# Kernel optimization log

Measured on AMD Instinct MI355X. Metric: run time of the kernel, lower is better.

The kernel has to match this reference:

```python
import jax, jax.numpy as jnp
import numpy as np

D_MODEL, H, D_FF = 1024, 16, 4096
D_K = D_MODEL // H
EPS = 1e-5


def _layernorm(x, alpha, bias):
    # faithful to source: unbiased std (ddof=1), eps added to std (not var)
    mean = jnp.mean(x, axis=-1, keepdims=True)
    std = jnp.std(x, axis=-1, keepdims=True, ddof=1)
    return alpha * (x - mean) / (std + EPS) + bias


def setup_inputs() -> dict:
    key = jax.random.key(0)
    ks = jax.random.split(key, 12)
    B, S = 2, 2048
    s = 1.0 / np.sqrt(D_MODEL)
    inp = {
        "x": jax.random.normal(ks[0], (B, S, D_MODEL), dtype=jnp.float32),
        "mask": jnp.ones((B, 1, 1, S), dtype=jnp.int32),
        "wq": jax.random.normal(ks[1], (D_MODEL, D_MODEL), dtype=jnp.float32) * s,
        "wk": jax.random.normal(ks[2], (D_MODEL, D_MODEL), dtype=jnp.float32) * s,
        "wv": jax.random.normal(ks[3], (D_MODEL, D_MODEL), dtype=jnp.float32) * s,
        "wo": jax.random.normal(ks[4], (D_MODEL, D_MODEL), dtype=jnp.float32) * s,
        "w1": jax.random.normal(ks[5], (D_MODEL, D_FF), dtype=jnp.float32) * s,
        "b1": jnp.zeros((D_FF,), dtype=jnp.float32),
        "w2": jax.random.normal(ks[6], (D_FF, D_MODEL), dtype=jnp.float32) * (1.0 / np.sqrt(D_FF)),
        "b2": jnp.zeros((D_MODEL,), dtype=jnp.float32),
        "alpha1": jnp.ones((1,), dtype=jnp.float32),
        "bias1": jnp.zeros((1,), dtype=jnp.float32),
        "alpha2": jnp.ones((1,), dtype=jnp.float32),
        "bias2": jnp.zeros((1,), dtype=jnp.float32),
    }
    return inp


def reference(x, mask, wq, wk, wv, wo, w1, b1, w2, b2, alpha1, bias1, alpha2, bias2):
    B, S, _ = x.shape

    # --- sublayer 1: pre-norm self-attention + residual ---
    xn = _layernorm(x, alpha1, bias1)
    q = (xn @ wq).reshape(B, S, H, D_K).transpose(0, 2, 1, 3)  # [B,H,S,Dk]
    k = (xn @ wk).reshape(B, S, H, D_K).transpose(0, 2, 1, 3)
    v = (xn @ wv).reshape(B, S, H, D_K).transpose(0, 2, 1, 3)

    scores = jnp.einsum("bhqd,bhkd->bhqk", q, k) / np.sqrt(D_K)  # [B,H,S,S]
    scores = jnp.where(mask == 0, jnp.float32(-1e9), scores)
    attn = jax.nn.softmax(scores, axis=-1)
    ctx = jnp.einsum("bhqk,bhkd->bhqd", attn, v)
    ctx = ctx.transpose(0, 2, 1, 3).reshape(B, S, D_MODEL)
    x = x + ctx @ wo

    # --- sublayer 2: pre-norm FFN + residual ---
    xn = _layernorm(x, alpha2, bias2)
    h = jax.nn.relu(xn @ w1 + b1)
    x = x + h @ w2 + b2
    return x
```

## Files before the change

kernel.cpp:

```cpp
#include <hip/hip_runtime.h>
#include <hip/hip_bf16.h>

typedef __attribute__((ext_vector_type(8))) short bf16x8;
typedef __attribute__((ext_vector_type(4))) short short4v;
typedef __attribute__((ext_vector_type(4))) float floatx4;

#define MFMA16(A, B, C) __builtin_amdgcn_mfma_f32_16x16x32_bf16((A), (B), (C), 0, 0, 0)

__device__ inline short bf16bits(float f) {
  __hip_bfloat16 h = __float2bfloat16(f);
  return *reinterpret_cast<short*>(&h);
}
__device__ inline unsigned cvtpk(float lo, float hi) {
  unsigned r;
  asm("v_cvt_pk_bf16_f32 %0, %1, %2" : "=v"(r) : "v"(lo), "v"(hi));
  return r;
}
typedef __attribute__((address_space(3))) char lds_char;
typedef __attribute__((address_space(1))) const char glob_char;
__device__ inline void gll16(const void* g, void* l) {
  __builtin_amdgcn_global_load_lds((glob_char*)g, (lds_char*)l, 16, 0, 0);
}

__global__ __launch_bounds__(256) void transpose_qkv_kernel(
    const float* __restrict__ wq, const float* __restrict__ wk,
    const float* __restrict__ wv, __hip_bfloat16* __restrict__ wqkvT) {
  __shared__ __align__(16) __hip_bfloat16 tile[64][72];
  const int which = blockIdx.y >> 4;
  const float* src = which == 0 ? wq : (which == 1 ? wk : wv);
  __hip_bfloat16* dst = wqkvT + (size_t)which * 1024 * 1024;
  const long r0 = (long)(blockIdx.y & 15) * 64, c0 = (long)blockIdx.x * 64;
  for (int i = threadIdx.x; i < 1024; i += 256) {
    int r = i >> 4, c4 = (i & 15) * 4;
    float4 f = *(const float4*)&src[(r0 + r) * 1024 + c0 + c4];
    short4v s;
    s[0] = bf16bits(f.x); s[1] = bf16bits(f.y);
    s[2] = bf16bits(f.z); s[3] = bf16bits(f.w);
    *(short4v*)&tile[r][c4] = s;
  }
  __syncthreads();
  for (int i = threadIdx.x; i < 512; i += 256) {
    int c = i >> 3, r8 = (i & 7) * 8;
    bf16x8 sv;
#pragma unroll
    for (int j = 0; j < 8; j++) sv[j] = *reinterpret_cast<const short*>(&tile[r8 + j][c]);
    *(bf16x8*)&dst[(c0 + c) * 1024 + r0 + r8] = sv;
  }
}

__global__ __launch_bounds__(256) void prep_kernel(
    const __hip_bfloat16* __restrict__ qkv, __hip_bfloat16* __restrict__ vt,
    const float* __restrict__ wo, __hip_bfloat16* __restrict__ woT,
    const int* __restrict__ mask, float* __restrict__ addm,
    int* __restrict__ flags) {
  __shared__ __align__(16) __hip_bfloat16 tile[64][72];
  __shared__ int ok[4];
  const int bid = blockIdx.x;
  if (bid < 1024) {
    const int bh = bid >> 5, b = bh >> 4, h = bh & 15;
    const long s0 = (long)(bid & 31) * 64;
    const __hip_bfloat16* src = qkv + ((long)b * 2048 + s0) * 3072 + 2048 + h * 64;
    for (int i = threadIdx.x; i < 512; i += 256) {
      int s = i >> 3, d8 = (i & 7) * 8;
      *(uint4*)&tile[s][d8] = *(const uint4*)&src[(long)s * 3072 + d8];
    }
    __syncthreads();
    __hip_bfloat16* dstb = vt + (long)bh * 64 * 2048 + s0;
    for (int i = threadIdx.x; i < 512; i += 256) {
      int d = i >> 3, s8 = (i & 7) * 8;
      bf16x8 sv;
#pragma unroll
      for (int j = 0; j < 8; j++) sv[j] = *reinterpret_cast<const short*>(&tile[s8 + j][d]);
      *(bf16x8*)&dstb[(long)d * 2048 + s8] = sv;
    }
  } else if (bid < 1280) {
    const int t = bid - 1024;
    const long r0 = (long)(t >> 4) * 64, c0 = (long)(t & 15) * 64;
    for (int i = threadIdx.x; i < 1024; i += 256) {
      int r = i >> 4, c4 = (i & 15) * 4;
      float4 f = *(const float4*)&wo[(r0 + r) * 1024 + c0 + c4];
      short4v s;
      s[0] = bf16bits(f.x); s[1] = bf16bits(f.y);
      s[2] = bf16bits(f.z); s[3] = bf16bits(f.w);
      *(short4v*)&tile[r][c4] = s;
    }
    __syncthreads();
    for (int i = threadIdx.x; i < 512; i += 256) {
      int c = i >> 3, r8 = (i & 7) * 8;
      bf16x8 sv;
#pragma unroll
      for (int j = 0; j < 8; j++) sv[j] = *reinterpret_cast<const short*>(&tile[r8 + j][c]);
      *(bf16x8*)&woT[(c0 + c) * 1024 + r0 + r8] = sv;
    }
  } else {
    const int i = (bid - 1280) * 256 + threadIdx.x;
    const int mv = mask[i];
    addm[i] = mv ? 0.f : -1e30f;
    const unsigned long long bal = __ballot(mv != 0);
    if ((threadIdx.x & 63) == 0) ok[threadIdx.x >> 6] = (bal == ~0ull) ? 1 : 0;
    __syncthreads();
    if (threadIdx.x == 0) flags[bid - 1280] = ok[0] & ok[1] & ok[2] & ok[3];
  }
}

__global__ __launch_bounds__(256) void wtrans_kernel(
    const float* __restrict__ w1c, const float* __restrict__ w2c,
    __hip_bfloat16* __restrict__ w1Th, __hip_bfloat16* __restrict__ w2Th) {
  __shared__ __align__(16) __hip_bfloat16 tile[64][72];
  const int bid = blockIdx.x;
  const float* src;
  __hip_bfloat16* dst;
  int R, ldS;
  long r0, c0;
  if (bid < 512) {
    src = w1c; dst = w1Th; R = 1024; ldS = 4096;
    r0 = (long)(bid >> 5) * 64; c0 = (long)(bid & 31) * 64;
  } else {
    const int t = bid - 512;
    src = w2c; dst = w2Th; R = 2048; ldS = 1024;
    r0 = (long)(t >> 4) * 64; c0 = (long)(t & 15) * 64;
  }
  for (int i = threadIdx.x; i < 1024; i += 256) {
    int r = i >> 4, c4 = (i & 15) * 4;
    float4 f = *(const float4*)&src[(r0 + r) * ldS + c0 + c4];
    short4v s;
    s[0] = bf16bits(f.x); s[1] = bf16bits(f.y);
    s[2] = bf16bits(f.z); s[3] = bf16bits(f.w);
    *(short4v*)&tile[r][c4] = s;
  }
  __syncthreads();
  for (int i = threadIdx.x; i < 512; i += 256) {
    int c = i >> 3, r8 = (i & 7) * 8;
    bf16x8 sv;
#pragma unroll
    for (int j = 0; j < 8; j++) sv[j] = *reinterpret_cast<const short*>(&tile[r8 + j][c]);
    *(bf16x8*)&dst[(c0 + c) * R + r0 + r8] = sv;
  }
}

__global__ __launch_bounds__(256) void bias_add_kernel(
    const float* __restrict__ x1, const float* __restrict__ b2,
    float* __restrict__ out) {
  const int i = (blockIdx.x * 256 + threadIdx.x) * 4;
  float4 v = *(const float4*)&x1[i];
  const float4 bb = *(const float4*)&b2[i & 1023];
  v.x += bb.x; v.y += bb.y; v.z += bb.z; v.w += bb.w;
  *(float4*)&out[i] = v;
}

__global__ __launch_bounds__(256) void ln_kernel(
    const float* __restrict__ x, __hip_bfloat16* __restrict__ y,
    const float* __restrict__ alpha_p, const float* __restrict__ bias_p) {
  __shared__ float sred[8];
  const long row = blockIdx.x;
  const int t = threadIdx.x;
  const float* xr = x + row * 1024;
  float v[4];
#pragma unroll
  for (int i = 0; i < 4; i++) v[i] = xr[t * 4 + i];
  float sum = 0.f, sq = 0.f;
#pragma unroll
  for (int i = 0; i < 4; i++) { sum += v[i]; sq += v[i] * v[i]; }
#pragma unroll
  for (int off = 32; off; off >>= 1) {
    sum += __shfl_down(sum, off);
    sq += __shfl_down(sq, off);
  }
  if ((t & 63) == 0) { sred[(t >> 6) * 2] = sum; sred[(t >> 6) * 2 + 1] = sq; }
  __syncthreads();
  sum = sred[0] + sred[2] + sred[4] + sred[6];
  sq = sred[1] + sred[3] + sred[5] + sred[7];
  const float mean = sum * (1.f / 1024.f);
  float var = (sq - 1024.f * mean * mean) * (1.f / 1023.f);
  var = fmaxf(var, 0.f);
  const float denom = sqrtf(var) + 1e-5f;
  const float sc = alpha_p[0] / denom;
  const float beta = bias_p[0];
  __hip_bfloat16* yr = y + row * 1024;
#pragma unroll
  for (int i = 0; i < 4; i++) yr[t * 4 + i] = __float2bfloat16((v[i] - mean) * sc + beta);
}

template <int EPI>
__global__ __launch_bounds__(256) void gemm_bt_kernel(
    const __hip_bfloat16* __restrict__ A, const __hip_bfloat16* __restrict__ Bt,
    void* __restrict__ Cv, const float* __restrict__ bias,
    const float* __restrict__ res, int M, int N, int K) {
  __shared__ __align__(16) __hip_bfloat16 lA[2][128 * 32];
  __shared__ __align__(16) __hip_bfloat16 lB[2][128 * 32];
  const int tid = threadIdx.x;
  const int wave = tid >> 6, lane = tid & 63;
  const int quad = lane >> 4, l16 = lane & 15;
  const int wm = wave >> 1, wn = wave & 1;

  const int gx = gridDim.x;
  const int nwg = gx * gridDim.y;
  int bid = blockIdx.y * gx + blockIdx.x;
  bid = (bid & 7) * (nwg >> 3) + (bid >> 3);
  const long m0 = (long)(bid / gx) * 128;
  const long n0 = (long)(bid % gx) * 128;

  const int rA0 = tid >> 2, cA0 = (tid & 3) * 8;
  const int rA1 = (tid + 256) >> 2, cA1 = ((tid + 256) & 3) * 8;

  floatx4 acc[4][4];
#pragma unroll
  for (int i = 0; i < 4; i++)
#pragma unroll
    for (int j = 0; j < 4; j++) acc[i][j] = (floatx4){0.f, 0.f, 0.f, 0.f};

  const __hip_bfloat16* Ab = A + m0 * K;
  const __hip_bfloat16* Bb = Bt + n0 * K;

  gll16(&Ab[(long)rA0 * K + cA0], &lA[0][wave * 512]);
  gll16(&Ab[(long)rA1 * K + cA1], &lA[0][2048 + wave * 512]);
  gll16(&Bb[(long)rA0 * K + cA0], &lB[0][wave * 512]);
  gll16(&Bb[(long)rA1 * K + cA1], &lB[0][2048 + wave * 512]);

  int cur = 0;
  for (int k0 = 0; k0 < K; k0 += 32) {
    __syncthreads();
    if (k0 + 32 < K) {
      const int nxt = cur ^ 1;
      gll16(&Ab[(long)rA0 * K + k0 + 32 + cA0], &lA[nxt][wave * 512]);
      gll16(&Ab[(long)rA1 * K + k0 + 32 + cA1], &lA[nxt][2048 + wave * 512]);
      gll16(&Bb[(long)rA0 * K + k0 + 32 + cA0], &lB[nxt][wave * 512]);
      gll16(&Bb[(long)rA1 * K + k0 + 32 + cA1], &lB[nxt][2048 + wave * 512]);
    }
    bf16x8 af[4], bfr[4];
#pragma unroll
    for (int mi = 0; mi < 4; mi++)
      af[mi] = *(const bf16x8*)&lA[cur][(wm * 64 + mi * 16 + l16) * 32 + quad * 8];
#pragma unroll
    for (int ni = 0; ni < 4; ni++)
      bfr[ni] = *(const bf16x8*)&lB[cur][(wn * 64 + ni * 16 + l16) * 32 + quad * 8];
#pragma unroll
    for (int mi = 0; mi < 4; mi++)
#pragma unroll
      for (int ni = 0; ni < 4; ni++)
        acc[mi][ni] = MFMA16(af[mi], bfr[ni], acc[mi][ni]);
    cur ^= 1;
  }

#pragma unroll
  for (int mi = 0; mi < 4; mi++) {
#pragma unroll
    for (int ni = 0; ni < 4; ni++) {
#pragma unroll
      for (int r = 0; r < 4; r++) {
        const long row = m0 + wm * 64 + mi * 16 + quad * 4 + r;
        const long col = n0 + wn * 64 + ni * 16 + l16;
        const long idx = row * N + col;
        float v = acc[mi][ni][r];
        if (EPI == 0) {
          ((__hip_bfloat16*)Cv)[idx] = __float2bfloat16(v);
        } else if (EPI == 1) {
          ((float*)Cv)[idx] = v + res[idx];
        } else if (EPI == 2) {
          v += bias[col];
          ((__hip_bfloat16*)Cv)[idx] = __float2bfloat16(fmaxf(v, 0.f));
        } else if (EPI == 3) {
          float* Cf = (float*)Cv;
          Cf[idx] = Cf[idx] + v;
        }
      }
    }
  }
}

template <int EPI>
__global__ __launch_bounds__(256) void gemm64_bt_kernel(
    const __hip_bfloat16* __restrict__ A, const __hip_bfloat16* __restrict__ Bt,
    void* __restrict__ Cv, const float* __restrict__ bias,
    const float* __restrict__ res, int M, int N, int K) {
  __shared__ __align__(16) __hip_bfloat16 lA[2][128 * 64];
  __shared__ __align__(16) __hip_bfloat16 lB[2][64 * 64];
  const int tid = threadIdx.x;
  const int wave = tid >> 6, lane = tid & 63;
  const int quad = lane >> 4, l16 = lane & 15;
  const int wm = wave >> 1, wn = wave & 1;

  const int gx = gridDim.x;
  const int nwg = gx * gridDim.y;
  int bid = blockIdx.y * gx + blockIdx.x;
  bid = (bid & 7) * (nwg >> 3) + (bid >> 3);
  const long m0 = (long)(bid / gx) * 128;
  const long n0 = (long)(bid % gx) * 64;

  const int srow = lane >> 3;
  const int cg = (lane & 7) ^ srow;

  floatx4 acc[4][2];
#pragma unroll
  for (int i = 0; i < 4; i++)
#pragma unroll
    for (int j = 0; j < 2; j++) acc[i][j] = (floatx4){0.f, 0.f, 0.f, 0.f};

  const __hip_bfloat16* Ab = A + m0 * K;
  const __hip_bfloat16* Bb = Bt + n0 * K;

#pragma unroll
  for (int j = 0; j < 4; ++j) {
    const int c = wave + j * 4;
    gll16(&Ab[(long)(c * 8 + srow) * K + cg * 8], &lA[0][c * 512]);
  }
#pragma unroll
  for (int j = 0; j < 2; ++j) {
    const int c = wave + j * 4;
    gll16(&Bb[(long)(c * 8 + srow) * K + cg * 8], &lB[0][c * 512]);
  }

  int cur = 0;
  for (int k0 = 0; k0 < K; k0 += 64) {
    __syncthreads();
    if (k0 + 64 < K) {
      const int nxt = cur ^ 1;
#pragma unroll
      for (int j = 0; j < 4; ++j) {
        const int c = wave + j * 4;
        gll16(&Ab[(long)(c * 8 + srow) * K + k0 + 64 + cg * 8], &lA[nxt][c * 512]);
      }
#pragma unroll
      for (int j = 0; j < 2; ++j) {
        const int c = wave + j * 4;
        gll16(&Bb[(long)(c * 8 + srow) * K + k0 + 64 + cg * 8], &lB[nxt][c * 512]);
      }
    }
#pragma unroll
    for (int ks = 0; ks < 2; ++ks) {
      bf16x8 af[4], bfr[2];
#pragma unroll
      for (int mi = 0; mi < 4; mi++) {
        const int row = wm * 64 + mi * 16 + l16;
        af[mi] = *(const bf16x8*)&lA[cur][row * 64 +
                                          (((ks * 4 + quad) ^ (l16 & 7)) * 8)];
      }
#pragma unroll
      for (int ni = 0; ni < 2; ni++) {
        const int row = wn * 32 + ni * 16 + l16;
        bfr[ni] = *(const bf16x8*)&lB[cur][row * 64 +
                                           (((ks * 4 + quad) ^ (l16 & 7)) * 8)];
      }
#pragma unroll
      for (int mi = 0; mi < 4; mi++)
#pragma unroll
        for (int ni = 0; ni < 2; ni++)
          acc[mi][ni] = MFMA16(af[mi], bfr[ni], acc[mi][ni]);
    }
    cur ^= 1;
  }

#pragma unroll
  for (int mi = 0; mi < 4; mi++) {
#pragma unroll
    for (int ni = 0; ni < 2; ni++) {
#pragma unroll
      for (int r = 0; r < 4; r++) {
        const long row = m0 + wm * 64 + mi * 16 + quad * 4 + r;
        const long col = n0 + wn * 32 + ni * 16 + l16;
        const long idx = row * N + col;
        float v = acc[mi][ni][r];
        if (EPI == 1) {
          ((float*)Cv)[idx] = v + res[idx];
        } else if (EPI == 3) {
          float* Cf = (float*)Cv;
          Cf[idx] = Cf[idx] + v;
        }
      }
    }
  }
}

__global__ __launch_bounds__(256) void attn_kernel(
    const __hip_bfloat16* __restrict__ qkv, const __hip_bfloat16* __restrict__ vt,
    const float* __restrict__ addm, const int* __restrict__ flags,
    __hip_bfloat16* __restrict__ ctx) {
  __shared__ __align__(16) __hip_bfloat16 lK[2][64 * 64];
  __shared__ __align__(16) __hip_bfloat16 lV[2][64 * 64];
  const int tid = threadIdx.x, wave = tid >> 6, lane = tid & 63;
  const int quad = lane >> 4, l16 = lane & 15;
  const int bh = blockIdx.y, b = bh >> 4, h = bh & 15;
  const int q0 = blockIdx.x * 64 + wave * 16;
  const float cs = 0.18033688011112042f;
  const float inv_cs = 5.545177444479562f;

  const __hip_bfloat16* kb = qkv + (long)b * 2048 * 3072 + 1024 + h * 64;
  const __hip_bfloat16* vb = vt + (long)bh * 64 * 2048;
  const float* am = addm + b * 2048;

  int fm = 1;
#pragma unroll
  for (int i = 0; i < 8; ++i) fm &= flags[b * 8 + i];
  const bool fast = (fm != 0);

  const long qoff = ((long)b * 2048 + q0 + l16) * 3072 + h * 64;
  const bf16x8 bq0 = *(const bf16x8*)&qkv[qoff + quad * 8];
  const bf16x8 bq1 = *(const bf16x8*)&qkv[qoff + 32 + quad * 8];

  const int srow = lane >> 3;
  const int cslot = lane & 7;
  const int cg = cslot ^ srow;
  const int rbase = wave * 16 + srow;

  floatx4 o[4];
#pragma unroll
  for (int mi = 0; mi < 4; mi++) o[mi] = (floatx4){0.f, 0.f, 0.f, 0.f};
  float mrow = 10.0f, lrow = 0.f;

#pragma unroll
  for (int j = 0; j < 2; ++j) {
    const int rloc = rbase + j * 8;
    gll16(kb + (long)rloc * 3072 + cg * 8, &lK[0][(wave * 16 + j * 8) * 64]);
    gll16(vb + (long)rloc * 2048 + cg * 8, &lV[0][(wave * 16 + j * 8) * 64]);
  }

  int cur = 0;
  for (int t = 0; t < 32; ++t) {
    __syncthreads();
    if (t + 1 < 32) {
      const int nxt = cur ^ 1;
#pragma unroll
      for (int j = 0; j < 2; ++j) {
        const int rloc = rbase + j * 8;
        gll16(kb + (long)((t + 1) * 64 + rloc) * 3072 + cg * 8,
              &lK[nxt][(wave * 16 + j * 8) * 64]);
        gll16(vb + (long)rloc * 2048 + (t + 1) * 64 + cg * 8,
              &lV[nxt][(wave * 16 + j * 8) * 64]);
      }
    }
    const __hip_bfloat16* lKc = lK[cur];
    const __hip_bfloat16* lVc = lV[cur];

    floatx4 c[4];
    __builtin_amdgcn_s_setprio(1);
#pragma unroll
    for (int g = 0; g < 4; ++g) {
      const bf16x8 a0 =
          *(const bf16x8*)&lKc[(g * 16 + l16) * 64 + ((quad) ^ (l16 & 7)) * 8];
      const bf16x8 a1 =
          *(const bf16x8*)&lKc[(g * 16 + l16) * 64 + ((4 + quad) ^ (l16 & 7)) * 8];
      floatx4 cc = {0.f, 0.f, 0.f, 0.f};
      cc = MFMA16(a0, bq0, cc);
      cc = MFMA16(a1, bq1, cc);
      c[g] = cc;
    }
    __builtin_amdgcn_s_setprio(0);

    if (!fast) {
#pragma unroll
      for (int g = 0; g < 4; ++g) {
        const float4 a4 = *(const float4*)&am[t * 64 + g * 16 + quad * 4];
        c[g][0] = fmaf(a4.x, inv_cs, c[g][0]);
        c[g][1] = fmaf(a4.y, inv_cs, c[g][1]);
        c[g][2] = fmaf(a4.z, inv_cs, c[g][2]);
        c[g][3] = fmaf(a4.w, inv_cs, c[g][3]);
      }
    }

    const float mneg = -mrow;
    float p[4][4];
#pragma unroll
    for (int g = 0; g < 4; ++g)
#pragma unroll
      for (int r = 0; r < 4; ++r)
        p[g][r] = __builtin_amdgcn_exp2f(fmaf(c[g][r], cs, mneg));

    const float m0 = fmaxf(fmaxf(c[0][0], c[0][1]), c[0][2]);
    const float m1 = fmaxf(fmaxf(c[0][3], c[1][0]), c[1][1]);
    const float m2 = fmaxf(fmaxf(c[1][2], c[1][3]), c[2][0]);
    const float m3 = fmaxf(fmaxf(c[2][1], c[2][2]), c[2][3]);
    const float m4 = fmaxf(fmaxf(c[3][0], c[3][1]), c[3][2]);
    float tm = fmaxf(fmaxf(fmaxf(m0, m1), fmaxf(m2, m3)), fmaxf(m4, c[3][3]));
    tm = fmaxf(tm, __shfl_xor(tm, 16));
    tm = fmaxf(tm, __shfl_xor(tm, 32));
    const float tms = tm * cs;

    const float s0 = (p[0][0] + p[0][1]) + (p[0][2] + p[0][3]);
    const float s1 = (p[1][0] + p[1][1]) + (p[1][2] + p[1][3]);
    const float s2 = (p[2][0] + p[2][1]) + (p[2][2] + p[2][3]);
    const float s3 = (p[3][0] + p[3][1]) + (p[3][2] + p[3][3]);
    float rs = (s0 + s1) + (s2 + s3);
    rs += __shfl_xor(rs, 16);
    rs += __shfl_xor(rs, 32);

    unsigned dw[4][2];
#pragma unroll
    for (int g = 0; g < 4; ++g) {
      dw[g][0] = cvtpk(p[g][0], p[g][1]);
      dw[g][1] = cvtpk(p[g][2], p[g][3]);
    }
    const int qs0 = (quad & 1) * 2;
    const int src0 = l16 + 16 * qs0, src1 = src0 + 16;
    const bool hig = (quad >> 1) != 0;
#pragma unroll
    for (int ss = 0; ss < 2; ++ss) {
      const unsigned a0 = __shfl((int)dw[2 * ss][0], src0);
      const unsigned b0 = __shfl((int)dw[2 * ss + 1][0], src0);
      const unsigned a1 = __shfl((int)dw[2 * ss][1], src0);
      const unsigned b1 = __shfl((int)dw[2 * ss + 1][1], src0);
      const unsigned a2 = __shfl((int)dw[2 * ss][0], src1);
      const unsigned b2 = __shfl((int)dw[2 * ss + 1][0], src1);
      const unsigned a3 = __shfl((int)dw[2 * ss][1], src1);
      const unsigned b3 = __shfl((int)dw[2 * ss + 1][1], src1);
      uint4 du;
      du.x = hig ? b0 : a0;
      du.y = hig ? b1 : a1;
      du.z = hig ? b2 : a2;
      du.w = hig ? b3 : a3;
      const bf16x8 bp = *reinterpret_cast<bf16x8*>(&du);
      __builtin_amdgcn_s_setprio(1);
#pragma unroll
      for (int mi = 0; mi < 4; ++mi) {
        const bf16x8 av = *(const bf16x8*)&lVc[(mi * 16 + l16) * 64 +
                                               ((ss * 4 + quad) ^ (l16 & 7)) * 8];
        o[mi] = MFMA16(av, bp, o[mi]);
      }
      __builtin_amdgcn_s_setprio(0);
    }

    lrow += rs;
    if (__any(tms > mrow + 8.f)) {
      const float mnew = fmaxf(mrow, tms);
      const float alpha = __builtin_amdgcn_exp2f(mrow - mnew);
      mrow = mnew;
      lrow *= alpha;
#pragma unroll
      for (int mi = 0; mi < 4; mi++) o[mi] *= alpha;
    }
    cur ^= 1;
  }

  const float inv_l = 1.f / lrow;
  const long cb = ((long)b * 2048 + q0 + l16) * 1024 + h * 64;
#pragma unroll
  for (int mi = 0; mi < 4; mi++) {
    uint2 st;
    st.x = cvtpk(o[mi][0] * inv_l, o[mi][1] * inv_l);
    st.y = cvtpk(o[mi][2] * inv_l, o[mi][3] * inv_l);
    *(uint2*)&ctx[cb + mi * 16 + quad * 4] = st;
  }
}

extern "C" void kernel_launch(void* const* d_in, const int* in_sizes, int n_in,
                              void* d_out, int out_size, void* d_ws, size_t ws_size,
                              hipStream_t stream) {
  const float* x = (const float*)d_in[0];
  const int* mask = (const int*)d_in[1];
  const float* wq = (const float*)d_in[2];
  const float* wk = (const float*)d_in[3];
  const float* wv = (const float*)d_in[4];
  const float* wo = (const float*)d_in[5];
  const float* w1 = (const float*)d_in[6];
  const float* b1 = (const float*)d_in[7];
  const float* w2 = (const float*)d_in[8];
  const float* b2 = (const float*)d_in[9];
  const float* alpha1 = (const float*)d_in[10];
  const float* bias1 = (const float*)d_in[11];
  const float* alpha2 = (const float*)d_in[12];
  const float* bias2 = (const float*)d_in[13];

  char* ws = (char*)d_ws;
  char* dob = (char*)d_out;
  const size_t MiB = 1048576;
  __hip_bfloat16* qkv   = (__hip_bfloat16*)(ws + 0);
  __hip_bfloat16* wqkvT = (__hip_bfloat16*)(ws + 24 * MiB);
  __hip_bfloat16* vtb   = (__hip_bfloat16*)(ws + 24 * MiB);
  float*          x1    = (float*)(ws + 0);
  __hip_bfloat16* hc    = (__hip_bfloat16*)(ws + 16 * MiB);
  __hip_bfloat16* xn    = (__hip_bfloat16*)d_out;
  __hip_bfloat16* ctxb  = (__hip_bfloat16*)d_out;
  __hip_bfloat16* xn2   = (__hip_bfloat16*)d_out;
  __hip_bfloat16* woT   = (__hip_bfloat16*)(dob + 8 * MiB);
  __hip_bfloat16* w1Th  = (__hip_bfloat16*)(dob + 8 * MiB);
  __hip_bfloat16* w2Th  = (__hip_bfloat16*)(dob + 12 * MiB);
  float*          addm  = (float*)(dob + 12 * MiB);
  int*            flags = (int*)(dob + 12 * MiB + 16 * 1024);

  const dim3 b256(256);
  transpose_qkv_kernel<<<dim3(16, 48), b256, 0, stream>>>(wq, wk, wv, wqkvT);
  ln_kernel<<<4096, b256, 0, stream>>>(x, xn, alpha1, bias1);
  gemm_bt_kernel<0><<<dim3(24, 32), b256, 0, stream>>>(xn, wqkvT, qkv, nullptr, nullptr,
                                                       4096, 3072, 1024);
  prep_kernel<<<1296, b256, 0, stream>>>(qkv, vtb, wo, woT, mask, addm, flags);
  attn_kernel<<<dim3(32, 32), b256, 0, stream>>>(qkv, vtb, addm, flags, ctxb);
  gemm64_bt_kernel<1><<<dim3(16, 32), b256, 0, stream>>>(ctxb, woT, x1, nullptr, x,
                                                         4096, 1024, 1024);
  ln_kernel<<<4096, b256, 0, stream>>>(x1, xn2, alpha2, bias2);
  for (int c = 0; c < 2; ++c) {
    wtrans_kernel<<<1024, b256, 0, stream>>>(w1 + c * 2048,
                                             w2 + (size_t)c * 2048 * 1024,
                                             w1Th, w2Th);
    gemm_bt_kernel<2><<<dim3(16, 32), b256, 0, stream>>>(xn2, w1Th, hc, b1 + c * 2048,
                                                         nullptr, 4096, 2048, 1024);
    gemm64_bt_kernel<3><<<dim3(16, 32), b256, 0, stream>>>(hc, w2Th, x1, nullptr,
                                                           nullptr, 4096, 1024, 2048);
  }
  bias_add_kernel<<<4096, b256, 0, stream>>>(x1, b2, (float*)d_out);
}
```

Before: 405.6 us.

## Fuse LN1 with QKV weight transpose, add K64 FFN1 GEMM, route P through LDS

Merges the first layernorm and the QKV weight transpose into one launch, with block index selecting the role, so one kernel launch goes away. Adds a GEMM variant with a 64-wide K step and 128x128 tiles, used for the first FFN matmul. In attention, the probability tile is packed to bf16 and written to a per-wave swizzled LDS buffer, then read back as the MFMA operand. This replaces the cross-lane shuffle-and-select sequence but adds LDS traffic and shared memory per block.

```diff
diff --git a/kernel.cpp b/kernel.cpp
--- a/kernel.cpp
+++ b/kernel.cpp
@@ -22,29 +22,63 @@
   __builtin_amdgcn_global_load_lds((glob_char*)g, (lds_char*)l, 16, 0, 0);
 }
 
-__global__ __launch_bounds__(256) void transpose_qkv_kernel(
+__global__ __launch_bounds__(256) void ln_qkvtrans_kernel(
+    const float* __restrict__ x, __hip_bfloat16* __restrict__ y,
+    const float* __restrict__ alpha_p, const float* __restrict__ bias_p,
     const float* __restrict__ wq, const float* __restrict__ wk,
     const float* __restrict__ wv, __hip_bfloat16* __restrict__ wqkvT) {
   __shared__ __align__(16) __hip_bfloat16 tile[64][72];
-  const int which = blockIdx.y >> 4;
-  const float* src = which == 0 ? wq : (which == 1 ? wk : wv);
-  __hip_bfloat16* dst = wqkvT + (size_t)which * 1024 * 1024;
-  const long r0 = (long)(blockIdx.y & 15) * 64, c0 = (long)blockIdx.x * 64;
-  for (int i = threadIdx.x; i < 1024; i += 256) {
-    int r = i >> 4, c4 = (i & 15) * 4;
-    float4 f = *(const float4*)&src[(r0 + r) * 1024 + c0 + c4];
-    short4v s;
-    s[0] = bf16bits(f.x); s[1] = bf16bits(f.y);
-    s[2] = bf16bits(f.z); s[3] = bf16bits(f.w);
-    *(short4v*)&tile[r][c4] = s;
-  }
-  __syncthreads();
-  for (int i = threadIdx.x; i < 512; i += 256) {
-    int c = i >> 3, r8 = (i & 7) * 8;
-    bf16x8 sv;
-#pragma unroll
-    for (int j = 0; j < 8; j++) sv[j] = *reinterpret_cast<const short*>(&tile[r8 + j][c]);
-    *(bf16x8*)&dst[(c0 + c) * 1024 + r0 + r8] = sv;
+  const int bid = blockIdx.x;
+  const int t = threadIdx.x;
+  if (bid < 4096) {
+    __shared__ float sred[8];
+    const float* xr = x + (long)bid * 1024;
+    float v[4];
+#pragma unroll
+    for (int i = 0; i < 4; i++) v[i] = xr[t * 4 + i];
+    float sum = 0.f, sq = 0.f;
+#pragma unroll
+    for (int i = 0; i < 4; i++) { sum += v[i]; sq += v[i] * v[i]; }
+#pragma unroll
+    for (int off = 32; off; off >>= 1) {
+      sum += __shfl_down(sum, off);
+      sq += __shfl_down(sq, off);
+    }
+    if ((t & 63) == 0) { sred[(t >> 6) * 2] = sum; sred[(t >> 6) * 2 + 1] = sq; }
+    __syncthreads();
+    sum = sred[0] + sred[2] + sred[4] + sred[6];
+    sq = sred[1] + sred[3] + sred[5] + sred[7];
+    const float mean = sum * (1.f / 1024.f);
+    float var = (sq - 1024.f * mean * mean) * (1.f / 1023.f);
+    var = fmaxf(var, 0.f);
+    const float denom = sqrtf(var) + 1e-5f;
+    const float sc = alpha_p[0] / denom;
+    const float beta = bias_p[0];
+    __hip_bfloat16* yr = y + (long)bid * 1024;
+#pragma unroll
+    for (int i = 0; i < 4; i++) yr[t * 4 + i] = __float2bfloat16((v[i] - mean) * sc + beta);
+  } else {
+    const int tt = bid - 4096;
+    const int which = tt >> 8;
+    const float* src = which == 0 ? wq : (which == 1 ? wk : wv);
+    __hip_bfloat16* dst = wqkvT + (size_t)which * 1024 * 1024;
+    const long r0 = (long)((tt >> 4) & 15) * 64, c0 = (long)(tt & 15) * 64;
+    for (int i = t; i < 1024; i += 256) {
+      int r = i >> 4, c4 = (i & 15) * 4;
+      float4 f = *(const float4*)&src[(r0 + r) * 1024 + c0 + c4];
+      short4v s;
+      s[0] = bf16bits(f.x); s[1] = bf16bits(f.y);
+      s[2] = bf16bits(f.z); s[3] = bf16bits(f.w);
+      *(short4v*)&tile[r][c4] = s;
+    }
+    __syncthreads();
+    for (int i = t; i < 512; i += 256) {
+      int c = i >> 3, r8 = (i & 7) * 8;
+      bf16x8 sv;
+#pragma unroll
+      for (int j = 0; j < 8; j++) sv[j] = *reinterpret_cast<const short*>(&tile[r8 + j][c]);
+      *(bf16x8*)&dst[(c0 + c) * 1024 + r0 + r8] = sv;
+    }
   }
 }
 
@@ -269,6 +303,106 @@
 }
 
 template <int EPI>
+__global__ __launch_bounds__(256) void gemm_bt_k64_kernel(
+    const __hip_bfloat16* __restrict__ A, const __hip_bfloat16* __restrict__ Bt,
+    void* __restrict__ Cv, const float* __restrict__ bias,
+    const float* __restrict__ res, int M, int N, int K) {
+  __shared__ __align__(16) __hip_bfloat16 lA[2][128 * 64];
+  __shared__ __align__(16) __hip_bfloat16 lB[2][128 * 64];
+  const int tid = threadIdx.x;
+  const int wave = tid >> 6, lane = tid & 63;
+  const int quad = lane >> 4, l16 = lane & 15;
+  const int wm = wave >> 1, wn = wave & 1;
+
+  const int gx = gridDim.x;
+  const int nwg = gx * gridDim.y;
+  int bid = blockIdx.y * gx + blockIdx.x;
+  bid = (bid & 7) * (nwg >> 3) + (bid >> 3);
+  const long m0 = (long)(bid / gx) * 128;
+  const long n0 = (long)(bid % gx) * 128;
+
+  const int srow = lane >> 3;
+  const int cg = (lane & 7) ^ srow;
+
+  floatx4 acc[4][4];
+#pragma unroll
+  for (int i = 0; i < 4; i++)
+#pragma unroll
+    for (int j = 0; j < 4; j++) acc[i][j] = (floatx4){0.f, 0.f, 0.f, 0.f};
+
+  const __hip_bfloat16* Ab = A + m0 * K;
+  const __hip_bfloat16* Bb = Bt + n0 * K;
+
+#pragma unroll
+  for (int j = 0; j < 4; ++j) {
+    const int c = wave + j * 4;
+    gll16(&Ab[(long)(c * 8 + srow) * K + cg * 8], &lA[0][c * 512]);
+    gll16(&Bb[(long)(c * 8 + srow) * K + cg * 8], &lB[0][c * 512]);
+  }
+
+  int cur = 0;
+  for (int k0 = 0; k0 < K; k0 += 64) {
+    __syncthreads();
+    if (k0 + 64 < K) {
+      const int nxt = cur ^ 1;
+#pragma unroll
+      for (int j = 0; j < 4; ++j) {
+        const int c = wave + j * 4;
+        gll16(&Ab[(long)(c * 8 + srow) * K + k0 + 64 + cg * 8], &lA[nxt][c * 512]);
+        gll16(&Bb[(long)(c * 8 + srow) * K + k0 + 64 + cg * 8], &lB[nxt][c * 512]);
+      }
+    }
+#pragma unroll
+    for (int ks = 0; ks < 2; ++ks) {
+      bf16x8 af[4], bfr[4];
+#pragma unroll
+      for (int mi = 0; mi < 4; mi++) {
+        const int row = wm * 64 + mi * 16 + l16;
+        af[mi] = *(const bf16x8*)&lA[cur][row * 64 +
+                                          (((ks * 4 + quad) ^ (l16 & 7)) * 8)];
+      }
+#pragma unroll
+      for (int ni = 0; ni < 4; ni++) {
+        const int row = wn * 64 + ni * 16 + l16;
+        bfr[ni] = *(const bf16x8*)&lB[cur][row * 64 +
+                                           (((ks * 4 + quad) ^ (l16 & 7)) * 8)];
+      }
+#pragma unroll
+      for (int mi = 0; mi < 4; mi++)
+#pragma unroll
+        for (int ni = 0; ni < 4; ni++)
+          acc[mi][ni] = MFMA16(af[mi], bfr[ni], acc[mi][ni]);
+    }
+    cur ^= 1;
+  }
+
+#pragma unroll
+  for (int mi = 0; mi < 4; mi++) {
+#pragma unroll
+    for (int ni = 0; ni < 4; ni++) {
+#pragma unroll
+      for (int r = 0; r < 4; r++) {
+        const long row = m0 + wm * 64 + mi * 16 + quad * 4 + r;
+        const long col = n0 + wn * 64 + ni * 16 + l16;
+        const long idx = row * N + col;
+        float v = acc[mi][ni][r];
+        if (EPI == 0) {
+          ((__hip_bfloat16*)Cv)[idx] = __float2bfloat16(v);
+        } else if (EPI == 1) {
+          ((float*)Cv)[idx] = v + res[idx];
+        } else if (EPI == 2) {
+          v += bias[col];
+          ((__hip_bfloat16*)Cv)[idx] = __float2bfloat16(fmaxf(v, 0.f));
+        } else if (EPI == 3) {
+          float* Cf = (float*)Cv;
+          Cf[idx] = Cf[idx] + v;
+        }
+      }
+    }
+  }
+}
+
+template <int EPI>
 __global__ __launch_bounds__(256) void gemm64_bt_kernel(
     const __hip_bfloat16* __restrict__ A, const __hip_bfloat16* __restrict__ Bt,
     void* __restrict__ Cv, const float* __restrict__ bias,
@@ -377,6 +511,7 @@
     __hip_bfloat16* __restrict__ ctx) {
   __shared__ __align__(16) __hip_bfloat16 lK[2][64 * 64];
   __shared__ __align__(16) __hip_bfloat16 lV[2][64 * 64];
+  __shared__ __align__(16) __hip_bfloat16 lP[4][16 * 64];
   const int tid = threadIdx.x, wave = tid >> 6, lane = tid & 63;
   const int quad = lane >> 4, l16 = lane & 15;
   const int bh = blockIdx.y, b = bh >> 4, h = bh & 15;
@@ -401,6 +536,10 @@
   const int cslot = lane & 7;
   const int cg = cslot ^ srow;
   const int rbase = wave * 16 + srow;
+
+  char* const pbase = (char*)&lP[wave][0];
+  const int prow = l16 * 128;
+  const int pswz = l16 & 7;
 
   floatx4 o[4];
 #pragma unroll
@@ -465,6 +604,15 @@
       for (int r = 0; r < 4; ++r)
         p[g][r] = __builtin_amdgcn_exp2f(fmaf(c[g][r], cs, mneg));
 
+#pragma unroll
+    for (int g = 0; g < 4; ++g) {
+      uint2 w2;
+      w2.x = cvtpk(p[g][0], p[g][1]);
+      w2.y = cvtpk(p[g][2], p[g][3]);
+      const int slot16 = (g * 2 + (quad >> 1)) ^ pswz;
+      *(uint2*)(pbase + prow + (slot16 << 4) + ((quad & 1) << 3)) = w2;
+    }
+
     const float m0 = fmaxf(fmaxf(c[0][0], c[0][1]), c[0][2]);
     const float m1 = fmaxf(fmaxf(c[0][3], c[1][0]), c[1][1]);
     const float m2 = fmaxf(fmaxf(c[1][2], c[1][3]), c[2][0]);
@@ -483,31 +631,10 @@
     rs += __shfl_xor(rs, 16);
     rs += __shfl_xor(rs, 32);
 
-    unsigned dw[4][2];
-#pragma unroll
-    for (int g = 0; g < 4; ++g) {
-      dw[g][0] = cvtpk(p[g][0], p[g][1]);
-      dw[g][1] = cvtpk(p[g][2], p[g][3]);
-    }
-    const int qs0 = (quad & 1) * 2;
-    const int src0 = l16 + 16 * qs0, src1 = src0 + 16;
-    const bool hig = (quad >> 1) != 0;
 #pragma unroll
     for (int ss = 0; ss < 2; ++ss) {
-      const unsigned a0 = __shfl((int)dw[2 * ss][0], src0);
-      const unsigned b0 = __shfl((int)dw[2 * ss + 1][0], src0);
-      const unsigned a1 = __shfl((int)dw[2 * ss][1], src0);
-      const unsigned b1 = __shfl((int)dw[2 * ss + 1][1], src0);
-      const unsigned a2 = __shfl((int)dw[2 * ss][0], src1);
-      const unsigned b2 = __shfl((int)dw[2 * ss + 1][0], src1);
-      const unsigned a3 = __shfl((int)dw[2 * ss][1], src1);
-      const unsigned b3 = __shfl((int)dw[2 * ss + 1][1], src1);
-      uint4 du;
-      du.x = hig ? b0 : a0;
-      du.y = hig ? b1 : a1;
-      du.z = hig ? b2 : a2;
-      du.w = hig ? b3 : a3;
-      const bf16x8 bp = *reinterpret_cast<bf16x8*>(&du);
+      const bf16x8 bp = *(const bf16x8*)(pbase + prow +
+                                         ((((ss << 2) + quad) ^ pswz) << 4));
       __builtin_amdgcn_s_setprio(1);
 #pragma unroll
       for (int mi = 0; mi < 4; ++mi) {
@@ -577,8 +704,8 @@
   int*            flags = (int*)(dob + 12 * MiB + 16 * 1024);
 
   const dim3 b256(256);
-  transpose_qkv_kernel<<<dim3(16, 48), b256, 0, stream>>>(wq, wk, wv, wqkvT);
-  ln_kernel<<<4096, b256, 0, stream>>>(x, xn, alpha1, bias1);
+  ln_qkvtrans_kernel<<<4864, b256, 0, stream>>>(x, xn, alpha1, bias1,
+                                                wq, wk, wv, wqkvT);
   gemm_bt_kernel<0><<<dim3(24, 32), b256, 0, stream>>>(xn, wqkvT, qkv, nullptr, nullptr,
                                                        4096, 3072, 1024);
   prep_kernel<<<1296, b256, 0, stream>>>(qkv, vtb, wo, woT, mask, addm, flags);
@@ -590,8 +717,9 @@
     wtrans_kernel<<<1024, b256, 0, stream>>>(w1 + c * 2048,
                                              w2 + (size_t)c * 2048 * 1024,
                                              w1Th, w2Th);
-    gemm_bt_kernel<2><<<dim3(16, 32), b256, 0, stream>>>(xn2, w1Th, hc, b1 + c * 2048,
-                                                         nullptr, 4096, 2048, 1024);
+    gemm_bt_k64_kernel<2><<<dim3(16, 32), b256, 0, stream>>>(xn2, w1Th, hc,
+                                                             b1 + c * 2048, nullptr,
+                                                             4096, 2048, 1024);
     gemm64_bt_kernel<3><<<dim3(16, 32), b256, 0, stream>>>(hc, w2Th, x1, nullptr,
                                                            nullptr, 4096, 1024, 2048);
   }
```

New measurement: 384.4 us. -5.2%, faster.
